# Kernel tuning notes

Measured on AMD Instinct MI355X. Metric: run time of the kernel, lower is better.

Reference implementation:

```python
import jax, jax.numpy as jnp
import numpy as np

N = 50000      # nodes
E = 1600000    # edges
IN = 128       # in_features
OUT = 64       # out_features
H = 2          # heads
ALPHA = 0.2    # LeakyReLU negative slope


def setup_inputs() -> dict:
    key = jax.random.key(0)
    k1, k2, k3, k4 = jax.random.split(key, 4)
    x = jax.random.normal(k1, (N, IN), dtype=jnp.float32)
    edge_index = jax.random.randint(k2, (2, E), 0, N, dtype=jnp.int32)
    # xavier-uniform-ish scaled params
    W = jax.random.normal(k3, (H, IN, OUT), dtype=jnp.float32) / np.float32(np.sqrt(IN))
    a = jax.random.normal(k4, (H, 2 * OUT, 1), dtype=jnp.float32) * np.float32(0.1)
    return {"x": x, "W": W, "a": a, "edge_index": edge_index}


def reference(x, W, a, edge_index):
    src = edge_index[0]
    dst = edge_index[1]
    # per-head linear transform: [N, H, O]
    Wh = jnp.einsum('ni,hio->nho', x, W)
    # split attention vector: a @ [Wh_i || Wh_j] == Wh_i@a_i + Wh_j@a_j
    a_i = a[:, :OUT, 0]   # [H, O]
    a_j = a[:, OUT:, 0]   # [H, O]
    s_i = jnp.einsum('nho,ho->nh', Wh, a_i)   # [N, H]
    s_j = jnp.einsum('nho,ho->nh', Wh, a_j)   # [N, H]
    # per-edge attention logits, LeakyReLU
    e = jax.nn.leaky_relu(s_i[src] + s_j[dst], negative_slope=ALPHA)  # [E, H]
    # faithful to source: GLOBAL softmax over all edges (dim=0) per head
    attn = jax.nn.softmax(e, axis=0)  # [E, H]
    # dropout with rate 0.0 -> identity (eval mode)
    msg = attn[:, :, None] * Wh[dst]  # [E, H, O]
    h = jax.ops.segment_sum(msg, dst, num_segments=N)  # [N, H, O]
    # concat heads along feature dim
    return h.reshape(N, H * OUT)
```

## Files before the change

kernel.cpp:

```cpp
#include <hip/hip_runtime.h>

#define NN 50000
#define EE 1600000
#define INF 128
#define OUTF 64
#define NH 2
#define ALPHA 0.2f

#define RNG 8
#define CHK 32
#define NPR (NN / RNG)
#define EPC (EE / CHK)


__global__ __launch_bounds__(128)
void gat_node(const float* __restrict__ x, const float* __restrict__ W,
              const float* __restrict__ a, float* __restrict__ out,
              float* __restrict__ si, float* __restrict__ sj,
              float* __restrict__ Z)
{
    __shared__ float Wl[INF * OUTF];
    const int h = blockIdx.x & 1;
    const int n0 = (blockIdx.x >> 1) * 128;

    {
        const float4* src = (const float4*)(W + h * (INF * OUTF));
        float4* dst = (float4*)Wl;
        #pragma unroll 4
        for (int k = threadIdx.x; k < (INF * OUTF) / 4; k += 128) dst[k] = src[k];
    }
    if (blockIdx.x == 0 && threadIdx.x < 2) Z[threadIdx.x] = 0.0f;

    const int tx = threadIdx.x & 7;
    const int ty = threadIdx.x >> 3;

    float ai[8], aj[8];
    #pragma unroll
    for (int c = 0; c < 8; ++c) {
        ai[c] = a[h * 2 * OUTF + tx * 8 + c];
        aj[c] = a[h * 2 * OUTF + OUTF + tx * 8 + c];
    }

    unsigned xoff[8];
    #pragma unroll
    for (int k = 0; k < 8; ++k) {
        int n = n0 + ty * 8 + k;
        if (n >= NN) n = NN - 1;
        xoff[k] = (unsigned)n * (INF * 4);
    }

    float acc[8][8];
    #pragma unroll
    for (int k = 0; k < 8; ++k)
        #pragma unroll
        for (int c = 0; c < 8; ++c) acc[k][c] = 0.0f;

    __syncthreads();

    const char* xc = (const char*)x;
    for (int i4 = 0; i4 < INF / 4; ++i4) {
        float4 xv[8];
        #pragma unroll
        for (int k = 0; k < 8; ++k)
            xv[k] = *(const float4*)(xc + xoff[k] + i4 * 16);

        float4 wa[4], wb[4];
        #pragma unroll
        for (int r = 0; r < 4; ++r) {
            const float* wrow = &Wl[(i4 * 4 + r) * OUTF + tx * 8];
            wa[r] = *(const float4*)(wrow);
            wb[r] = *(const float4*)(wrow + 4);
        }
        #pragma unroll
        for (int k = 0; k < 8; ++k) {
            const float* xk = (const float*)&xv[k];
            #pragma unroll
            for (int r = 0; r < 4; ++r) {
                const float xs = xk[r];
                acc[k][0] = fmaf(xs, wa[r].x, acc[k][0]);
                acc[k][1] = fmaf(xs, wa[r].y, acc[k][1]);
                acc[k][2] = fmaf(xs, wa[r].z, acc[k][2]);
                acc[k][3] = fmaf(xs, wa[r].w, acc[k][3]);
                acc[k][4] = fmaf(xs, wb[r].x, acc[k][4]);
                acc[k][5] = fmaf(xs, wb[r].y, acc[k][5]);
                acc[k][6] = fmaf(xs, wb[r].z, acc[k][6]);
                acc[k][7] = fmaf(xs, wb[r].w, acc[k][7]);
            }
        }
    }

    #pragma unroll
    for (int k = 0; k < 8; ++k) {
        float pi = 0.0f, pj = 0.0f;
        #pragma unroll
        for (int c = 0; c < 8; ++c) {
            pi = fmaf(acc[k][c], ai[c], pi);
            pj = fmaf(acc[k][c], aj[c], pj);
        }
        #pragma unroll
        for (int m = 1; m < 8; m <<= 1) {
            pi += __shfl_xor(pi, m, 64);
            pj += __shfl_xor(pj, m, 64);
        }
        const int n = n0 + ty * 8 + k;
        if (n < NN) {
            if (tx == 0) {
                si[2 * n + h] = pi;
                sj[2 * n + h] = pj;
            }
            float4* o4 = (float4*)(out + (size_t)n * (NH * OUTF) + h * OUTF + tx * 8);
            o4[0] = make_float4(acc[k][0], acc[k][1], acc[k][2], acc[k][3]);
            o4[1] = make_float4(acc[k][4], acc[k][5], acc[k][6], acc[k][7]);
        }
    }
}

__global__ __launch_bounds__(512)
void gat_hist(const int* __restrict__ ei, const float* __restrict__ si,
              const float* __restrict__ sj, float* __restrict__ partial,
              float* __restrict__ Z)
{
    __shared__ float bins[NPR * 2];
    __shared__ float zr0[8], zr1[8];
    const int r = blockIdx.x / CHK;
    const int c = blockIdx.x % CHK;
    const int nlo = r * NPR;

    {
        float4* b4 = (float4*)bins;
        #pragma unroll 4
        for (int i = threadIdx.x; i < NPR * 2 / 4; i += 512)
            b4[i] = make_float4(0.f, 0.f, 0.f, 0.f);
    }
    __syncthreads();

    const int ebase = c * EPC;
    float z0 = 0.0f, z1 = 0.0f;

    for (int i = threadIdx.x; i < EPC / 4; i += 512) {
        const int4 s4 = *(const int4*)&ei[ebase + 4 * i];
        const int4 d4 = *(const int4*)&ei[EE + ebase + 4 * i];
        const int ss[4] = {s4.x, s4.y, s4.z, s4.w};
        const int dd[4] = {d4.x, d4.y, d4.z, d4.w};
        #pragma unroll
        for (int k = 0; k < 4; ++k) {
            const unsigned rel = (unsigned)(dd[k] - nlo);
            if (rel < NPR) {
                const float2 vi = *(const float2*)&si[2 * ss[k]];
                const float2 vj = *(const float2*)&sj[2 * dd[k]];
                float a0 = vi.x + vj.x; a0 = a0 > 0.0f ? a0 : ALPHA * a0;
                float a1 = vi.y + vj.y; a1 = a1 > 0.0f ? a1 : ALPHA * a1;
                const float w0 = expf(a0);
                const float w1 = expf(a1);
                atomicAdd(&bins[2 * rel], w0);
                atomicAdd(&bins[2 * rel + 1], w1);
                z0 += w0; z1 += w1;
            }
        }
    }

    #pragma unroll
    for (int m = 1; m < 64; m <<= 1) {
        z0 += __shfl_xor(z0, m, 64);
        z1 += __shfl_xor(z1, m, 64);
    }
    const int wv = threadIdx.x >> 6;
    if ((threadIdx.x & 63) == 0) { zr0[wv] = z0; zr1[wv] = z1; }
    __syncthreads();
    if (threadIdx.x == 0) {
        float t0 = 0.f, t1 = 0.f;
        #pragma unroll
        for (int i = 0; i < 8; ++i) { t0 += zr0[i]; t1 += zr1[i]; }
        atomicAdd(&Z[0], t0);
        atomicAdd(&Z[1], t1);
    }

    float* P = partial + (size_t)c * 100000 + nlo * 2;
    const float4* b4 = (const float4*)bins;
    #pragma unroll 4
    for (int i = threadIdx.x; i < NPR * 2 / 4; i += 512)
        ((float4*)P)[i] = b4[i];
}

__global__ __launch_bounds__(256)
void gat_sum(const float* __restrict__ partial, float* __restrict__ cf,
             const float* __restrict__ Z)
{
    const int i = blockIdx.x * 256 + threadIdx.x;
    if (i >= 100000 / 4) return;
    float4 s = make_float4(0.f, 0.f, 0.f, 0.f);
    #pragma unroll 8
    for (int c = 0; c < CHK; ++c) {
        const float4 v = ((const float4*)(partial + (size_t)c * 100000))[i];
        s.x += v.x; s.y += v.y; s.z += v.z; s.w += v.w;
    }
    const float r0 = 1.0f / Z[0], r1 = 1.0f / Z[1];
    s.x *= r0; s.y *= r1; s.z *= r0; s.w *= r1;
    ((float4*)cf)[i] = s;
}

__global__ __launch_bounds__(256)
void gat_final(float* __restrict__ out, const float* __restrict__ cf)
{
    const int total4 = NN * NH * OUTF / 4;
    const int idx = blockIdx.x * 256 + threadIdx.x;
    if (idx >= total4) return;
    const int base = idx << 2;
    const int n = base >> 7;
    const int h = (base >> 6) & 1;
    const float scale = cf[2 * n + h];
    float4* p = (float4*)out + idx;
    float4 v = *p;
    v.x *= scale; v.y *= scale; v.z *= scale; v.w *= scale;
    *p = v;
}

extern "C" void kernel_launch(void* const* d_in, const int* in_sizes, int n_in,
                              void* d_out, int out_size, void* d_ws, size_t ws_size,
                              hipStream_t stream)
{
    const float* x = (const float*)d_in[0];
    const float* W = (const float*)d_in[1];
    const float* a = (const float*)d_in[2];
    const int* ei = (const int*)d_in[3];
    float* out = (float*)d_out;
    float* ws = (float*)d_ws;

    float* si = ws;
    float* sj = ws + 100000;
    float* cf = ws + 200000;
    float* Z = ws + 300000;
    float* partial = ws + 300008;

    const int tiles = (NN + 127) / 128;
    gat_node<<<dim3(tiles * NH), dim3(128), 0, stream>>>(x, W, a, out, si, sj, Z);

    gat_hist<<<dim3(RNG * CHK), dim3(512), 0, stream>>>(ei, si, sj, partial, Z);

    gat_sum<<<dim3((100000 / 4 + 255) / 256), dim3(256), 0, stream>>>(partial, cf, Z);

    const int fblocks = (NN * NH * OUTF / 4 + 255) / 256;
    gat_final<<<dim3(fblocks), dim3(256), 0, stream>>>(out, cf);
}
```

Baseline: 169.6 us.

## Use split-bf16 MFMA for node transform and retune histogram partitioning

Rewrites the node linear transform to use bf16 MFMA instructions, splitting fp32 inputs into hi/lo bf16 parts (three MFMAs per tile) to keep near-fp32 accuracy, with W pre-swizzled into LDS for both heads in a single block. The histogram kernel now uses 16 node ranges with smaller LDS bins and up to 64 edge chunks chosen from workspace size, passed as runtime parameters. The aim is to cut FMA-bound GEMM time and raise occupancy in the scatter stage, at the cost of more partial-sum traffic and some accuracy loss from the split-bf16 approximation.

New measurement: 182.1 us. 1.07x slower.

```diff
diff --git a/kernel.cpp b/kernel.cpp
--- a/kernel.cpp
+++ b/kernel.cpp
@@ -7,110 +7,143 @@
 #define NH 2
 #define ALPHA 0.2f
 
-#define RNG 8
-#define CHK 32
+#define RNG 16
 #define NPR (NN / RNG)
-#define EPC (EE / CHK)
-
-
-__global__ __launch_bounds__(128)
-void gat_node(const float* __restrict__ x, const float* __restrict__ W,
+
+typedef __attribute__((ext_vector_type(8))) short s16x8;
+typedef __attribute__((ext_vector_type(4))) float f32x4;
+
+__device__ __forceinline__ unsigned short bf16_rne(float f) {
+    union { float f; unsigned u; } v; v.f = f;
+    unsigned r = v.u + 0x7FFFu + ((v.u >> 16) & 1u);
+    return (unsigned short)(r >> 16);
+}
+__device__ __forceinline__ float bf16_val(unsigned short h) {
+    union { unsigned u; float f; } v; v.u = ((unsigned)h) << 16;
+    return v.f;
+}
+__device__ __forceinline__ void split8(const float4 a, const float4 b,
+                                       s16x8& hi, s16x8& lo) {
+    const float p[8] = {a.x, a.y, a.z, a.w, b.x, b.y, b.z, b.w};
+    #pragma unroll
+    for (int j = 0; j < 8; ++j) {
+        const unsigned short h = bf16_rne(p[j]);
+        hi[j] = (short)h;
+        lo[j] = (short)bf16_rne(p[j] - bf16_val(h));
+    }
+}
+
+
+__global__ __launch_bounds__(256)
+void gat_node(const float* __restrict__ x, const float* __restrict__ Wg,
               const float* __restrict__ a, float* __restrict__ out,
               float* __restrict__ si, float* __restrict__ sj,
               float* __restrict__ Z)
 {
-    __shared__ float Wl[INF * OUTF];
-    const int h = blockIdx.x & 1;
-    const int n0 = (blockIdx.x >> 1) * 128;
-
-    {
-        const float4* src = (const float4*)(W + h * (INF * OUTF));
-        float4* dst = (float4*)Wl;
-        #pragma unroll 4
-        for (int k = threadIdx.x; k < (INF * OUTF) / 4; k += 128) dst[k] = src[k];
-    }
-    if (blockIdx.x == 0 && threadIdx.x < 2) Z[threadIdx.x] = 0.0f;
-
-    const int tx = threadIdx.x & 7;
-    const int ty = threadIdx.x >> 3;
-
-    float ai[8], aj[8];
-    #pragma unroll
-    for (int c = 0; c < 8; ++c) {
-        ai[c] = a[h * 2 * OUTF + tx * 8 + c];
-        aj[c] = a[h * 2 * OUTF + OUTF + tx * 8 + c];
-    }
-
-    unsigned xoff[8];
-    #pragma unroll
-    for (int k = 0; k < 8; ++k) {
-        int n = n0 + ty * 8 + k;
-        if (n >= NN) n = NN - 1;
-        xoff[k] = (unsigned)n * (INF * 4);
-    }
-
-    float acc[8][8];
-    #pragma unroll
-    for (int k = 0; k < 8; ++k)
-        #pragma unroll
-        for (int c = 0; c < 8; ++c) acc[k][c] = 0.0f;
+    __shared__ unsigned short Wf[2 * 16384];
+    const int tid = threadIdx.x;
+
+    for (int idx = tid; idx < 16384; idx += 256) {
+        const int h = idx >> 13;
+        const int k = (idx >> 6) & 127;
+        const int o = idx & 63;
+        const float w = Wg[idx];
+        const unsigned short hi = bf16_rne(w);
+        const unsigned short lo = bf16_rne(w - bf16_val(hi));
+        const int n  = h * 64 + o;
+        const int nt = n >> 4;
+        const int ks = k >> 5;
+        const int kk = k & 31;
+        const int ln = (kk >> 3) * 16 + (n & 15);
+        const int pos = ((nt * 4 + ks) * 64 + ln) * 8 + (kk & 7);
+        Wf[pos] = hi;
+        Wf[16384 + pos] = lo;
+    }
+    if (blockIdx.x == 0 && tid < 2) Z[tid] = 0.0f;
+
+    const int lane = tid & 63;
+    const int wv = tid >> 6;
+    const int lm = lane & 15;
+    const int quad = lane >> 4;
+
+    float aiv[8], ajv[8];
+    #pragma unroll
+    for (int nt = 0; nt < 8; ++nt) {
+        const int h = nt >> 2;
+        const int o = (nt * 16 + lm) & 63;
+        aiv[nt] = a[h * 128 + o];
+        ajv[nt] = a[h * 128 + 64 + o];
+    }
+
+    const int rowA0 = blockIdx.x * 128 + wv * 32 + lm;
+    const int rowA1 = rowA0 + 16;
+    const int rc0 = rowA0 < NN ? rowA0 : NN - 1;
+    const int rc1 = rowA1 < NN ? rowA1 : NN - 1;
+    const float* xp0 = x + (size_t)rc0 * INF + quad * 8;
+    const float* xp1 = x + (size_t)rc1 * INF + quad * 8;
+
+    f32x4 acc[2][8];
+    #pragma unroll
+    for (int mi = 0; mi < 2; ++mi)
+        #pragma unroll
+        for (int nt = 0; nt < 8; ++nt) acc[mi][nt] = (f32x4)0.0f;
 
     __syncthreads();
 
-    const char* xc = (const char*)x;
-    for (int i4 = 0; i4 < INF / 4; ++i4) {
-        float4 xv[8];
-        #pragma unroll
-        for (int k = 0; k < 8; ++k)
-            xv[k] = *(const float4*)(xc + xoff[k] + i4 * 16);
-
-        float4 wa[4], wb[4];
+    #pragma unroll
+    for (int ks = 0; ks < 4; ++ks) {
+        s16x8 ah0, al0, ah1, al1;
+        {
+            const float4 u0 = *(const float4*)(xp0 + ks * 32);
+            const float4 v0 = *(const float4*)(xp0 + ks * 32 + 4);
+            split8(u0, v0, ah0, al0);
+            const float4 u1 = *(const float4*)(xp1 + ks * 32);
+            const float4 v1 = *(const float4*)(xp1 + ks * 32 + 4);
+            split8(u1, v1, ah1, al1);
+        }
+        #pragma unroll
+        for (int nt = 0; nt < 8; ++nt) {
+            const s16x8 bh = *(const s16x8*)&Wf[((nt * 4 + ks) * 64 + lane) * 8];
+            const s16x8 bl = *(const s16x8*)&Wf[16384 + ((nt * 4 + ks) * 64 + lane) * 8];
+            acc[0][nt] = __builtin_amdgcn_mfma_f32_16x16x32_bf16(ah0, bh, acc[0][nt], 0, 0, 0);
+            acc[0][nt] = __builtin_amdgcn_mfma_f32_16x16x32_bf16(ah0, bl, acc[0][nt], 0, 0, 0);
+            acc[0][nt] = __builtin_amdgcn_mfma_f32_16x16x32_bf16(al0, bh, acc[0][nt], 0, 0, 0);
+            acc[1][nt] = __builtin_amdgcn_mfma_f32_16x16x32_bf16(ah1, bh, acc[1][nt], 0, 0, 0);
+            acc[1][nt] = __builtin_amdgcn_mfma_f32_16x16x32_bf16(ah1, bl, acc[1][nt], 0, 0, 0);
+            acc[1][nt] = __builtin_amdgcn_mfma_f32_16x16x32_bf16(al1, bh, acc[1][nt], 0, 0, 0);
+        }
+    }
+
+    #pragma unroll
+    for (int mi = 0; mi < 2; ++mi) {
+        const int rowb = blockIdx.x * 128 + wv * 32 + mi * 16 + quad * 4;
         #pragma unroll
         for (int r = 0; r < 4; ++r) {
-            const float* wrow = &Wl[(i4 * 4 + r) * OUTF + tx * 8];
-            wa[r] = *(const float4*)(wrow);
-            wb[r] = *(const float4*)(wrow + 4);
-        }
-        #pragma unroll
-        for (int k = 0; k < 8; ++k) {
-            const float* xk = (const float*)&xv[k];
+            const int rr = rowb + r;
+            float pi0 = 0.f, pi1 = 0.f, pj0 = 0.f, pj1 = 0.f;
             #pragma unroll
-            for (int r = 0; r < 4; ++r) {
-                const float xs = xk[r];
-                acc[k][0] = fmaf(xs, wa[r].x, acc[k][0]);
-                acc[k][1] = fmaf(xs, wa[r].y, acc[k][1]);
-                acc[k][2] = fmaf(xs, wa[r].z, acc[k][2]);
-                acc[k][3] = fmaf(xs, wa[r].w, acc[k][3]);
-                acc[k][4] = fmaf(xs, wb[r].x, acc[k][4]);
-                acc[k][5] = fmaf(xs, wb[r].y, acc[k][5]);
-                acc[k][6] = fmaf(xs, wb[r].z, acc[k][6]);
-                acc[k][7] = fmaf(xs, wb[r].w, acc[k][7]);
-            }
-        }
-    }
-
-    #pragma unroll
-    for (int k = 0; k < 8; ++k) {
-        float pi = 0.0f, pj = 0.0f;
-        #pragma unroll
-        for (int c = 0; c < 8; ++c) {
-            pi = fmaf(acc[k][c], ai[c], pi);
-            pj = fmaf(acc[k][c], aj[c], pj);
-        }
-        #pragma unroll
-        for (int m = 1; m < 8; m <<= 1) {
-            pi += __shfl_xor(pi, m, 64);
-            pj += __shfl_xor(pj, m, 64);
-        }
-        const int n = n0 + ty * 8 + k;
-        if (n < NN) {
-            if (tx == 0) {
-                si[2 * n + h] = pi;
-                sj[2 * n + h] = pj;
-            }
-            float4* o4 = (float4*)(out + (size_t)n * (NH * OUTF) + h * OUTF + tx * 8);
-            o4[0] = make_float4(acc[k][0], acc[k][1], acc[k][2], acc[k][3]);
-            o4[1] = make_float4(acc[k][4], acc[k][5], acc[k][6], acc[k][7]);
+            for (int nt = 0; nt < 4; ++nt) {
+                pi0 = fmaf(acc[mi][nt][r],     aiv[nt],     pi0);
+                pj0 = fmaf(acc[mi][nt][r],     ajv[nt],     pj0);
+                pi1 = fmaf(acc[mi][nt + 4][r], aiv[nt + 4], pi1);
+                pj1 = fmaf(acc[mi][nt + 4][r], ajv[nt + 4], pj1);
+            }
+            #pragma unroll
+            for (int m = 1; m < 16; m <<= 1) {
+                pi0 += __shfl_xor(pi0, m, 64);
+                pi1 += __shfl_xor(pi1, m, 64);
+                pj0 += __shfl_xor(pj0, m, 64);
+                pj1 += __shfl_xor(pj1, m, 64);
+            }
+            if (rr < NN) {
+                if (lm == 0) {
+                    si[2 * rr] = pi0; si[2 * rr + 1] = pi1;
+                    sj[2 * rr] = pj0; sj[2 * rr + 1] = pj1;
+                }
+                float* orow = out + (size_t)rr * (NH * OUTF) + lm;
+                #pragma unroll
+                for (int nt = 0; nt < 8; ++nt) orow[nt * 16] = acc[mi][nt][r];
+            }
         }
     }
 }
@@ -118,26 +151,27 @@
 __global__ __launch_bounds__(512)
 void gat_hist(const int* __restrict__ ei, const float* __restrict__ si,
               const float* __restrict__ sj, float* __restrict__ partial,
-              float* __restrict__ Z)
+              float* __restrict__ Z, const int epc)
 {
     __shared__ float bins[NPR * 2];
     __shared__ float zr0[8], zr1[8];
-    const int r = blockIdx.x / CHK;
-    const int c = blockIdx.x % CHK;
+    const int c = blockIdx.x;
+    const int r = blockIdx.y;
     const int nlo = r * NPR;
 
     {
-        float4* b4 = (float4*)bins;
-        #pragma unroll 4
-        for (int i = threadIdx.x; i < NPR * 2 / 4; i += 512)
-            b4[i] = make_float4(0.f, 0.f, 0.f, 0.f);
+        float2* b2 = (float2*)bins;
+        #pragma unroll 2
+        for (int i = threadIdx.x; i < NPR; i += 512)
+            b2[i] = make_float2(0.f, 0.f);
     }
     __syncthreads();
 
-    const int ebase = c * EPC;
+    const int ebase = c * epc;
+    const int ng = epc >> 2;
     float z0 = 0.0f, z1 = 0.0f;
 
-    for (int i = threadIdx.x; i < EPC / 4; i += 512) {
+    for (int i = threadIdx.x; i < ng; i += 512) {
         const int4 s4 = *(const int4*)&ei[ebase + 4 * i];
         const int4 d4 = *(const int4*)&ei[EE + ebase + 4 * i];
         const int ss[4] = {s4.x, s4.y, s4.z, s4.w};
@@ -175,22 +209,22 @@
         atomicAdd(&Z[1], t1);
     }
 
-    float* P = partial + (size_t)c * 100000 + nlo * 2;
-    const float4* b4 = (const float4*)bins;
-    #pragma unroll 4
-    for (int i = threadIdx.x; i < NPR * 2 / 4; i += 512)
-        ((float4*)P)[i] = b4[i];
+    float2* P = (float2*)(partial + (size_t)c * 100000 + nlo * 2);
+    const float2* b2 = (const float2*)bins;
+    #pragma unroll 2
+    for (int i = threadIdx.x; i < NPR; i += 512)
+        P[i] = b2[i];
 }
 
 __global__ __launch_bounds__(256)
 void gat_sum(const float* __restrict__ partial, float* __restrict__ cf,
-             const float* __restrict__ Z)
+             const float* __restrict__ Z, const int chk)
 {
     const int i = blockIdx.x * 256 + threadIdx.x;
     if (i >= 100000 / 4) return;
     float4 s = make_float4(0.f, 0.f, 0.f, 0.f);
     #pragma unroll 8
-    for (int c = 0; c < CHK; ++c) {
+    for (int c = 0; c < chk; ++c) {
         const float4 v = ((const float4*)(partial + (size_t)c * 100000))[i];
         s.x += v.x; s.y += v.y; s.z += v.z; s.w += v.w;
     }
@@ -230,14 +264,18 @@
     float* sj = ws + 100000;
     float* cf = ws + 200000;
     float* Z = ws + 300000;
-    float* partial = ws + 300008;
+    float* partial = ws + 300016;
+
+    const size_t avail_f = ws_size / 4;
+    const int chk = (avail_f >= 300016UL + 64UL * 100000UL) ? 64 : 32;
+    const int epc = EE / chk;
 
     const int tiles = (NN + 127) / 128;
-    gat_node<<<dim3(tiles * NH), dim3(128), 0, stream>>>(x, W, a, out, si, sj, Z);
-
-    gat_hist<<<dim3(RNG * CHK), dim3(512), 0, stream>>>(ei, si, sj, partial, Z);
-
-    gat_sum<<<dim3((100000 / 4 + 255) / 256), dim3(256), 0, stream>>>(partial, cf, Z);
+    gat_node<<<dim3(tiles), dim3(256), 0, stream>>>(x, W, a, out, si, sj, Z);
+
+    gat_hist<<<dim3(chk, RNG), dim3(512), 0, stream>>>(ei, si, sj, partial, Z, epc);
+
+    gat_sum<<<dim3((100000 / 4 + 255) / 256), dim3(256), 0, stream>>>(partial, cf, Z, chk);
 
     const int fblocks = (NN * NH * OUTF / 4 + 255) / 256;
     gat_final<<<dim3(fblocks), dim3(256), 0, stream>>>(out, cf);
```
